# Performance work log

Hardware: AMD Instinct MI355X
Metric: run time of the kernel (lower is better)

Reference implementation:

```python
import jax, jax.numpy as jnp
import numpy as np

N = 100000
E = 3_200_000
H = 64
R = 2
NEG = 0.01   # leaky_relu default slope
EPS = 1e-5   # BatchNorm eps


def leaky(x):
    return jnp.where(x > 0, x, NEG * x)


def bn(x, g, b, m, v):
    # BatchNorm1d in eval mode (running statistics)
    return (x - m) * jax.lax.rsqrt(v + EPS) * g + b


def setup_inputs() -> dict:
    key = jax.random.key(0)
    ks = jax.random.split(key, 16)
    d = {}
    d["des"] = jax.random.normal(ks[0], (N, 768), jnp.float32)
    d["num"] = jax.random.normal(ks[1], (N, 5), jnp.float32)
    d["cat"] = jax.random.normal(ks[2], (N, 6), jnp.float32)
    d["edge_index"] = jax.random.randint(ks[3], (2, E), 0, N)
    d["edge_type"] = jax.random.randint(ks[4], (E,), 0, R)

    def lin(k, o, i):
        return (jax.random.normal(k, (o, i), jnp.float32) / np.float32(np.sqrt(i)))

    # projection heads: Linear + BatchNorm1d params
    d["des_W"] = lin(ks[5], H, 768); d["des_b"] = jnp.zeros((H,), jnp.float32)
    d["num_W"] = lin(ks[6], H, 5);   d["num_b"] = jnp.zeros((H,), jnp.float32)
    d["cat_W"] = lin(ks[7], H, 6);   d["cat_b"] = jnp.zeros((H,), jnp.float32)
    for name, kk in (("des", ks[8]), ("num", ks[9]), ("cat", ks[10])):
        d[name + "_g"] = jnp.ones((H,), jnp.float32)
        d[name + "_beta"] = jnp.zeros((H,), jnp.float32)
        d[name + "_m"] = 0.1 * jax.random.normal(kk, (H,), jnp.float32)
        d[name + "_v"] = jnp.ones((H,), jnp.float32)
    # RGCN relation weights [R, in, out] (used as F.linear(x, W[r]) -> x @ W[r].T)
    d["rgcn_W"] = jax.random.normal(ks[11], (R, H, H), jnp.float32) / np.float32(np.sqrt(H))
    # classifier
    d["cls_W1"] = lin(ks[12], H // 2, H); d["cls_b1"] = jnp.zeros((H // 2,), jnp.float32)
    d["cls_W2"] = lin(ks[13], 2, H // 2); d["cls_b2"] = jnp.zeros((2,), jnp.float32)
    return d


def reference(des, num, cat, edge_index, edge_type,
              des_W, des_b, des_g, des_beta, des_m, des_v,
              num_W, num_b, num_g, num_beta, num_m, num_v,
              cat_W, cat_b, cat_g, cat_beta, cat_m, cat_v,
              rgcn_W, cls_W1, cls_b1, cls_W2, cls_b2):
    # feature fusion: three Linear+BN+LeakyReLU branches summed
    x = leaky(bn(des @ des_W.T + des_b, des_g, des_beta, des_m, des_v))
    x = x + leaky(bn(num @ num_W.T + num_b, num_g, num_beta, num_m, num_v))
    x = x + leaky(bn(cat @ cat_W.T + cat_b, cat_g, cat_beta, cat_m, cat_v))

    # SimpleRGCNConv: per-relation linear transform + masked scatter-mean over edges
    src, dst = edge_index[0], edge_index[1]  # PyG: row=source, col=target
    n = x.shape[0]
    acc = jnp.zeros((n, H), x.dtype)
    for r in range(R):
        x_r = x @ rgcn_W[r].T                       # F.linear(x, weight[r])
        mask = (edge_type == r).astype(x.dtype)     # [E]
        msg = x_r[src] * mask[:, None]              # gather + mask
        s = jax.ops.segment_sum(msg, dst, num_segments=n)
        cnt = jax.ops.segment_sum(mask, dst, num_segments=n)
        acc = acc + s / jnp.maximum(cnt, 1.0)[:, None]  # mean; 0 for isolated nodes
    x = leaky(acc / R)  # mean over relations

    # dropout in eval mode is identity; classifier
    h = leaky(x @ cls_W1.T + cls_b1)
    return h @ cls_W2.T + cls_b2
```

## Files before the change

### kernel.cpp

```cpp
#include <hip/hip_runtime.h>

typedef unsigned int u32;
typedef unsigned short u16;

#define NEG 0.01f
#define BN_EPS 1e-5f

typedef __attribute__((ext_vector_type(8))) short bf16x8;
typedef __attribute__((ext_vector_type(4))) float f32x4;

__device__ __forceinline__ float bl(u32 u){ union { u32 i; float f; } c; c.i = u << 16; return c.f; }
__device__ __forceinline__ float bh(u32 u){ union { u32 i; float f; } c; c.i = u & 0xFFFF0000u; return c.f; }
__device__ __forceinline__ u16 f2b(float f){
  union { float f; u32 i; } c; c.f = f;
  u32 t = c.i + 0x7FFFu + ((c.i >> 16) & 1u);
  return (u16)(t >> 16);
}
__device__ __forceinline__ float leaky(float v){ return v > 0.f ? v : NEG * v; }

__global__ __launch_bounds__(256) void k_hist_prep(
    const int* __restrict__ ei, const int* __restrict__ et, int E, int HB,
    int* __restrict__ deg2,
    const float* __restrict__ desWf, const float* __restrict__ rgcnW,
    const float* __restrict__ W1, u16* __restrict__ tab)
{
  int bid = blockIdx.x;
  if (bid < HB) {
    int e = bid * 256 + threadIdx.x;
    if (e < E) atomicAdd(&deg2[ei[E + e] * 2 + et[e]], 1);
  } else {
    int i = (bid - HB) * 256 + threadIdx.x;
    if (i < 49152) {
      int j = i & 7, lane = (i >> 3) & 63, t = (i >> 9) & 3, k = i >> 11;
      int row = 16 * t + (lane & 15);
      int col = 32 * k + 8 * (lane >> 4) + j;
      tab[i] = f2b(desWf[row * 768 + col]);
    } else if (i < 57344) {
      int j = i - 49152;
      int h = j >> 7, k = j & 127;
      tab[i] = f2b(rgcnW[(k >= 64 ? 4096 : 0) + h * 64 + (k & 63)]);
    } else if (i < 59392) {
      tab[i] = f2b(W1[i - 57344]);
    }
  }
}

__global__ __launch_bounds__(256) void k_fuse_scan(
    const float* __restrict__ des, const float* __restrict__ nump, const float* __restrict__ catp,
    const u16* __restrict__ Wpk, const float* __restrict__ desB,
    const float* __restrict__ numW, const float* __restrict__ numB,
    const float* __restrict__ catW, const float* __restrict__ catB,
    const float* __restrict__ dg, const float* __restrict__ dbe, const float* __restrict__ dm, const float* __restrict__ dv,
    const float* __restrict__ ng, const float* __restrict__ nbe, const float* __restrict__ nm, const float* __restrict__ nv,
    const float* __restrict__ cg, const float* __restrict__ cbe, const float* __restrict__ cm, const float* __restrict__ cv,
    u16* __restrict__ x16, int n,
    const int* __restrict__ deg2, int* __restrict__ offs2, int M)
{
  const int tid  = threadIdx.x;
  const int lane = tid & 63;
  const int w    = tid >> 6;

  if (blockIdx.x == 0) {
    __shared__ int wsum[4];
    __shared__ int carry;
    if (tid == 0) carry = 0;
    __syncthreads();
    for (int base = 0; base < M; base += 1024) {
      int idx = base + tid * 4;
      int4 v = {0, 0, 0, 0};
      if (idx < M) v = *(const int4*)(deg2 + idx);
      int s4 = v.x + v.y + v.z + v.w;
      int s = s4;
      #pragma unroll
      for (int o = 1; o < 64; o <<= 1) { int t = __shfl_up(s, o); if (lane >= o) s += t; }
      if (lane == 63) wsum[w] = s;
      __syncthreads();
      if (tid == 0) {
        int a = wsum[0];
        a += wsum[1]; wsum[1] = a;
        a += wsum[2]; wsum[2] = a;
        a += wsum[3]; wsum[3] = a;
      }
      __syncthreads();
      int wbase = (w == 0) ? 0 : wsum[w - 1];
      int ebase = carry + wbase + (s - s4);
      if (idx < M) {
        int4 o4;
        o4.x = ebase;
        o4.y = ebase + v.x;
        o4.z = ebase + v.x + v.y;
        o4.w = ebase + v.x + v.y + v.z;
        *(int4*)(offs2 + idx) = o4;
      }
      __syncthreads();
      if (tid == 0) carry += wsum[3];
      __syncthreads();
    }
    if (tid == 0) offs2[M] = carry;
    return;
  }

  __shared__ float ync[64][66];
  __shared__ __align__(16) u16 atile[64 * 136];

  const int quad = lane >> 4;
  const int l15  = lane & 15;
  const int fb   = blockIdx.x - 1;
  const int rowbase = fb * 64 + 16 * w;

  {
    float nw[5], cw[6];
    #pragma unroll
    for (int j = 0; j < 5; ++j) nw[j] = numW[lane * 5 + j];
    #pragma unroll
    for (int j = 0; j < 6; ++j) cw[j] = catW[lane * 6 + j];
    float An = ng[lane] * rsqrtf(nv[lane] + BN_EPS);
    float Bn = (numB[lane] - nm[lane]) * An + nbe[lane];
    float Ac = cg[lane] * rsqrtf(cv[lane] + BN_EPS);
    float Bc = (catB[lane] - cm[lane]) * Ac + cbe[lane];
    for (int m = 0; m < 16; ++m) {
      int node = rowbase + m; if (node > n - 1) node = n - 1;
      float yn = 0.f, yc = 0.f;
      #pragma unroll
      for (int j = 0; j < 5; ++j) yn = fmaf(nump[node * 5 + j], nw[j], yn);
      #pragma unroll
      for (int j = 0; j < 6; ++j) yc = fmaf(catp[node * 6 + j], cw[j], yc);
      ync[16 * w + m][lane] = leaky(yn * An + Bn) + leaky(yc * Ac + Bc);
    }
  }

  float Ad4[4], Bd4[4];
  #pragma unroll
  for (int t = 0; t < 4; ++t) {
    int nn = 16 * t + l15;
    float A = dg[nn] * rsqrtf(dv[nn] + BN_EPS);
    Ad4[t] = A;
    Bd4[t] = (desB[nn] - dm[nn]) * A + dbe[nn];
  }
  __syncthreads();

  const u16* bP = Wpk + lane * 8;

  f32x4 acc[4];
  #pragma unroll
  for (int t = 0; t < 4; ++t) acc[t] = (f32x4){0.f, 0.f, 0.f, 0.f};

  const int blk64 = fb * 64;
  for (int tile = 0; tile < 6; ++tile) {
    if (tile > 0) __syncthreads();
    #pragma unroll
    for (int it = 0; it < 4; ++it) {
      int j  = it * 256 + tid;
      int r  = j >> 4;
      int sg = j & 15;
      int row = blk64 + r; if (row > n - 1) row = n - 1;
      const float* p = des + (size_t)row * 768 + tile * 128 + sg * 8;
      float4 u = *(const float4*)p;
      float4 v = *(const float4*)(p + 4);
      u32* d = (u32*)(atile + r * 136 + sg * 8);
      d[0] = (u32)f2b(u.x) | ((u32)f2b(u.y) << 16);
      d[1] = (u32)f2b(u.z) | ((u32)f2b(u.w) << 16);
      d[2] = (u32)f2b(v.x) | ((u32)f2b(v.y) << 16);
      d[3] = (u32)f2b(v.z) | ((u32)f2b(v.w) << 16);
    }
    __syncthreads();
    #pragma unroll
    for (int kk = 0; kk < 4; ++kk) {
      bf16x8 a = *(const bf16x8*)(atile + (16 * w + l15) * 136 + kk * 32 + quad * 8);
      int kg = tile * 4 + kk;
      acc[0] = __builtin_amdgcn_mfma_f32_16x16x32_bf16(a, *(const bf16x8*)(bP + kg * 2048       ), acc[0], 0, 0, 0);
      acc[1] = __builtin_amdgcn_mfma_f32_16x16x32_bf16(a, *(const bf16x8*)(bP + kg * 2048 +  512), acc[1], 0, 0, 0);
      acc[2] = __builtin_amdgcn_mfma_f32_16x16x32_bf16(a, *(const bf16x8*)(bP + kg * 2048 + 1024), acc[2], 0, 0, 0);
      acc[3] = __builtin_amdgcn_mfma_f32_16x16x32_bf16(a, *(const bf16x8*)(bP + kg * 2048 + 1536), acc[3], 0, 0, 0);
    }
  }

  #pragma unroll
  for (int t = 0; t < 4; ++t) {
    #pragma unroll
    for (int r = 0; r < 4; ++r) {
      int m = quad * 4 + r;
      int node = rowbase + m;
      if (node < n) {
        int nn = 16 * t + l15;
        float v = leaky(acc[t][r] * Ad4[t] + Bd4[t]) + ync[16 * w + m][nn];
        x16[(size_t)node * 64 + nn] = f2b(v);
      }
    }
  }
}

__global__ void k_place(const int* __restrict__ ei, const int* __restrict__ et, int E,
                        const int* __restrict__ offs2, int* __restrict__ cur2, int* __restrict__ packed)
{
  int e = blockIdx.x * 256 + threadIdx.x;
  if (e < E) {
    int bin = ei[E + e] * 2 + et[e];
    int pos = offs2[bin] + atomicAdd(&cur2[bin], 1);
    packed[pos] = ei[e];
  }
}

__global__ __launch_bounds__(256) void k_agg(
    const u16* __restrict__ x16, const int* __restrict__ offs2, const int* __restrict__ packed,
    u32* __restrict__ agg, int n)
{
  const int tid = threadIdx.x, lane = tid & 63, w = tid >> 6;
  const int c = lane & 31, half = lane >> 5;

  for (int nd = blockIdx.x * 4 + w; nd < n; nd += gridDim.x * 4) {
    int o0 = offs2[nd * 2], o1 = offs2[nd * 2 + 1], o2 = offs2[nd * 2 + 2];
    float aE[2], aO[2];

    #pragma unroll
    for (int rel = 0; rel < 2; ++rel) {
      int beg = rel ? o1 : o0;
      int end = rel ? o2 : o1;
      float accE = 0.f, accO = 0.f;
      for (int j0 = beg; j0 < end; j0 += 64) {
        int idx = j0 + lane;
        int p = (idx < end) ? packed[idx] : 0;
        p = (p < 0) ? 0 : ((p > n - 1) ? (n - 1) : p);
        int cn = end - j0; if (cn > 64) cn = 64;
        int t = 0;
        for (; t + 16 <= cn; t += 16) {
          int s0 = __shfl(p, t      + half);
          int s1 = __shfl(p, t + 2  + half);
          int s2 = __shfl(p, t + 4  + half);
          int s3 = __shfl(p, t + 6  + half);
          int s4 = __shfl(p, t + 8  + half);
          int s5 = __shfl(p, t + 10 + half);
          int s6 = __shfl(p, t + 12 + half);
          int s7 = __shfl(p, t + 14 + half);
          u32 v0 = *(const u32*)(x16 + (size_t)s0 * 64 + 2 * c);
          u32 v1 = *(const u32*)(x16 + (size_t)s1 * 64 + 2 * c);
          u32 v2 = *(const u32*)(x16 + (size_t)s2 * 64 + 2 * c);
          u32 v3 = *(const u32*)(x16 + (size_t)s3 * 64 + 2 * c);
          u32 v4 = *(const u32*)(x16 + (size_t)s4 * 64 + 2 * c);
          u32 v5 = *(const u32*)(x16 + (size_t)s5 * 64 + 2 * c);
          u32 v6 = *(const u32*)(x16 + (size_t)s6 * 64 + 2 * c);
          u32 v7 = *(const u32*)(x16 + (size_t)s7 * 64 + 2 * c);
          accE += ((bl(v0) + bl(v1)) + (bl(v2) + bl(v3))) + ((bl(v4) + bl(v5)) + (bl(v6) + bl(v7)));
          accO += ((bh(v0) + bh(v1)) + (bh(v2) + bh(v3))) + ((bh(v4) + bh(v5)) + (bh(v6) + bh(v7)));
        }
        for (; t + 8 <= cn; t += 8) {
          int s0 = __shfl(p, t     + half);
          int s1 = __shfl(p, t + 2 + half);
          int s2 = __shfl(p, t + 4 + half);
          int s3 = __shfl(p, t + 6 + half);
          u32 v0 = *(const u32*)(x16 + (size_t)s0 * 64 + 2 * c);
          u32 v1 = *(const u32*)(x16 + (size_t)s1 * 64 + 2 * c);
          u32 v2 = *(const u32*)(x16 + (size_t)s2 * 64 + 2 * c);
          u32 v3 = *(const u32*)(x16 + (size_t)s3 * 64 + 2 * c);
          accE += (bl(v0) + bl(v1)) + (bl(v2) + bl(v3));
          accO += (bh(v0) + bh(v1)) + (bh(v2) + bh(v3));
        }
        for (; t + 2 <= cn; t += 2) {
          int s0 = __shfl(p, t + half);
          u32 v0 = *(const u32*)(x16 + (size_t)s0 * 64 + 2 * c);
          accE += bl(v0); accO += bh(v0);
        }
        if (t < cn) {
          int s0 = __shfl(p, t);
          if (half == 0) {
            u32 v0 = *(const u32*)(x16 + (size_t)s0 * 64 + 2 * c);
            accE += bl(v0); accO += bh(v0);
          }
        }
      }
      accE += __shfl_xor(accE, 32);
      accO += __shfl_xor(accO, 32);
      int cnt = end - beg;
      float sc = 1.f / (float)(cnt > 1 ? cnt : 1);
      aE[rel] = accE * sc;
      aO[rel] = accO * sc;
    }

    float sE = half ? aE[1] : aE[0];
    float sO = half ? aO[1] : aO[0];
    agg[(size_t)nd * 64 + lane] = (u32)f2b(sE) | ((u32)f2b(sO) << 16);
  }
}

__global__ __launch_bounds__(256) void k_mlp(
    const u32* __restrict__ agg, const u16* __restrict__ Wmlp, const u16* __restrict__ W1p,
    const float* __restrict__ b1, const float* __restrict__ W2, const float* __restrict__ b2,
    float2* __restrict__ out, int n)
{
  __shared__ __align__(16) u16 h1[4][16][72];
  __shared__ float h2[4][16][34];

  const int tid = threadIdx.x, lane = tid & 63, w = tid >> 6;
  const int quad = lane >> 4, l15 = lane & 15;
  const int rowbase = blockIdx.x * 64 + 16 * w;

  int rowA = rowbase + l15; if (rowA > n - 1) rowA = n - 1;
  const u16* aRow = (const u16*)(agg + (size_t)rowA * 64);

  f32x4 acc[4];
  #pragma unroll
  for (int t = 0; t < 4; ++t) acc[t] = (f32x4){0.f, 0.f, 0.f, 0.f};
  #pragma unroll
  for (int ks = 0; ks < 4; ++ks) {
    bf16x8 a = *(const bf16x8*)(aRow + ks * 32 + quad * 8);
    #pragma unroll
    for (int t = 0; t < 4; ++t) {
      bf16x8 b = *(const bf16x8*)(Wmlp + (size_t)(16 * t + l15) * 128 + ks * 32 + quad * 8);
      acc[t] = __builtin_amdgcn_mfma_f32_16x16x32_bf16(a, b, acc[t], 0, 0, 0);
    }
  }
  #pragma unroll
  for (int t = 0; t < 4; ++t)
    #pragma unroll
    for (int r = 0; r < 4; ++r) {
      int m = quad * 4 + r;
      h1[w][m][16 * t + l15] = f2b(leaky(0.5f * acc[t][r]));
    }
  __syncthreads();

  f32x4 acc2[2];
  acc2[0] = (f32x4){0.f, 0.f, 0.f, 0.f};
  acc2[1] = (f32x4){0.f, 0.f, 0.f, 0.f};
  #pragma unroll
  for (int ks = 0; ks < 2; ++ks) {
    bf16x8 a = *(const bf16x8*)(&h1[w][l15][ks * 32 + quad * 8]);
    #pragma unroll
    for (int t = 0; t < 2; ++t) {
      bf16x8 b = *(const bf16x8*)(W1p + (size_t)(16 * t + l15) * 64 + ks * 32 + quad * 8);
      acc2[t] = __builtin_amdgcn_mfma_f32_16x16x32_bf16(a, b, acc2[t], 0, 0, 0);
    }
  }
  #pragma unroll
  for (int t = 0; t < 2; ++t)
    #pragma unroll
    for (int r = 0; r < 4; ++r) {
      int m = quad * 4 + r;
      int j = 16 * t + l15;
      h2[w][m][j] = leaky(acc2[t][r] + b1[j]);
    }
  __syncthreads();

  float t0 = 0.f, t1 = 0.f;
  #pragma unroll
  for (int jj = 0; jj < 8; ++jj) {
    int j = quad * 8 + jj;
    float hv = h2[w][l15][j];
    t0 = fmaf(hv, W2[j], t0);
    t1 = fmaf(hv, W2[32 + j], t1);
  }
  t0 += __shfl_xor(t0, 16); t0 += __shfl_xor(t0, 32);
  t1 += __shfl_xor(t1, 16); t1 += __shfl_xor(t1, 32);
  int node = rowbase + l15;
  if (quad == 0 && node < n) {
    float2 q; q.x = t0 + b2[0]; q.y = t1 + b2[1];
    out[node] = q;
  }
}

extern "C" void kernel_launch(void* const* d_in, const int* in_sizes, int n_in,
                              void* d_out, int out_size, void* d_ws, size_t ws_size,
                              hipStream_t stream)
{
  const float* des  = (const float*)d_in[0];
  const float* nump = (const float*)d_in[1];
  const float* catp = (const float*)d_in[2];
  const int* ei   = (const int*)d_in[3];
  const int* et   = (const int*)d_in[4];
  const float* desW = (const float*)d_in[5];
  const float* desB = (const float*)d_in[6];
  const float* numW = (const float*)d_in[7];
  const float* numB = (const float*)d_in[8];
  const float* catW = (const float*)d_in[9];
  const float* catB = (const float*)d_in[10];
  const float* dg  = (const float*)d_in[11];
  const float* dbe = (const float*)d_in[12];
  const float* dm  = (const float*)d_in[13];
  const float* dv  = (const float*)d_in[14];
  const float* ng  = (const float*)d_in[15];
  const float* nbe = (const float*)d_in[16];
  const float* nm  = (const float*)d_in[17];
  const float* nv  = (const float*)d_in[18];
  const float* cg  = (const float*)d_in[19];
  const float* cbe = (const float*)d_in[20];
  const float* cm  = (const float*)d_in[21];
  const float* cv  = (const float*)d_in[22];
  const float* rgcnW = (const float*)d_in[23];
  const float* W1 = (const float*)d_in[24];
  const float* b1 = (const float*)d_in[25];
  const float* W2 = (const float*)d_in[26];
  const float* b2 = (const float*)d_in[27];

  const int N = in_sizes[1] / 5;
  const int E = in_sizes[4];
  const int M = 2 * N;
  const int NB = (N + 63) / 64;

  char* ws = (char*)d_ws;
  u16* tab    = (u16*)ws;                  size_t off = (size_t)59392 * 2;
  off = (off + 255) & ~(size_t)255;
  u16* x16    = (u16*)(ws + off);          off += (size_t)N * 64 * 2;
  u32* agg    = (u32*)(ws + off);          off += (size_t)N * 64 * 4;
  int* deg2   = (int*)(ws + off);          off += (size_t)M * 4;
  int* cur2   = (int*)(ws + off);          off += (size_t)M * 4;
  int* offs2  = (int*)(ws + off);          off += (size_t)(M + 1) * 4;
  off = (off + 255) & ~(size_t)255;
  int* packed = (int*)(ws + off);

  u16* Wpk    = tab;
  u16* Wmlp   = tab + 49152;
  u16* W1p    = tab + 57344;

  hipMemsetAsync(deg2, 0, (size_t)M * 8, stream);

  const int HB = (E + 255) / 256;
  const int PB = (59392 + 255) / 256;
  k_hist_prep<<<HB + PB, 256, 0, stream>>>(ei, et, E, HB, deg2, desW, rgcnW, W1, tab);

  k_fuse_scan<<<NB + 1, 256, 0, stream>>>(des, nump, catp, Wpk, desB, numW, numB, catW, catB,
                                          dg, dbe, dm, dv, ng, nbe, nm, nv, cg, cbe, cm, cv,
                                          x16, N, deg2, offs2, M);

  k_place<<<(E + 255) / 256, 256, 0, stream>>>(ei, et, E, offs2, cur2, packed);
  k_agg<<<2048, 256, 0, stream>>>(x16, offs2, packed, agg, N);
  k_mlp<<<(N + 63) / 64, 256, 0, stream>>>(agg, Wmlp, W1p, b1, W2, b2, (float2*)d_out, N);
}
```

Baseline: 942.0 us.

## Replace single-block serial scan with three-pass multi-block prefix scan

The exclusive prefix scan over per-node, per-relation degree counts used to run in one block that loops serially over 200K entries alongside the fuse kernel. It is now split into three kernels: per-chunk reduction, a single-block scan of the chunk sums, and a per-chunk scan that adds the offsets. This removes a long single-block tail, at the cost of two extra launches and losing overlap with the fuse work. NCH is 196, which fits inside the 256-thread scanB.

```diff
diff --git a/kernel.cpp b/kernel.cpp
--- a/kernel.cpp
+++ b/kernel.cpp
@@ -45,7 +45,80 @@
   }
 }
 
-__global__ __launch_bounds__(256) void k_fuse_scan(
+__global__ __launch_bounds__(256) void k_scanA(
+    const int* __restrict__ deg2, int* __restrict__ psum, int M)
+{
+  __shared__ int ws4[4];
+  const int tid = threadIdx.x, lane = tid & 63, w = tid >> 6;
+  int idx = blockIdx.x * 1024 + tid * 4;
+  int4 v = {0, 0, 0, 0};
+  if (idx < M) v = *(const int4*)(deg2 + idx);
+  int s = v.x + v.y + v.z + v.w;
+  #pragma unroll
+  for (int o = 1; o < 64; o <<= 1) s += __shfl_xor(s, o);
+  if (lane == 0) ws4[w] = s;
+  __syncthreads();
+  if (tid == 0) psum[blockIdx.x] = ws4[0] + ws4[1] + ws4[2] + ws4[3];
+}
+
+__global__ __launch_bounds__(256) void k_scanB(
+    const int* __restrict__ psum, int* __restrict__ poff, int NCH)
+{
+  __shared__ int wsum[4];
+  const int tid = threadIdx.x, lane = tid & 63, w = tid >> 6;
+  int v = (tid < NCH) ? psum[tid] : 0;
+  int s = v;
+  #pragma unroll
+  for (int o = 1; o < 64; o <<= 1) { int t = __shfl_up(s, o); if (lane >= o) s += t; }
+  if (lane == 63) wsum[w] = s;
+  __syncthreads();
+  if (tid == 0) {
+    int a = wsum[0];
+    a += wsum[1]; wsum[1] = a;
+    a += wsum[2]; wsum[2] = a;
+    a += wsum[3]; wsum[3] = a;
+  }
+  __syncthreads();
+  int wbase = (w == 0) ? 0 : wsum[w - 1];
+  if (tid < NCH) poff[tid] = wbase + (s - v);
+}
+
+__global__ __launch_bounds__(256) void k_scanC(
+    const int* __restrict__ deg2, const int* __restrict__ poff,
+    int* __restrict__ offs2, int M, int E)
+{
+  __shared__ int wsum[4];
+  const int tid = threadIdx.x, lane = tid & 63, w = tid >> 6;
+  int idx = blockIdx.x * 1024 + tid * 4;
+  int4 v = {0, 0, 0, 0};
+  if (idx < M) v = *(const int4*)(deg2 + idx);
+  int s4 = v.x + v.y + v.z + v.w;
+  int s = s4;
+  #pragma unroll
+  for (int o = 1; o < 64; o <<= 1) { int t = __shfl_up(s, o); if (lane >= o) s += t; }
+  if (lane == 63) wsum[w] = s;
+  __syncthreads();
+  if (tid == 0) {
+    int a = wsum[0];
+    a += wsum[1]; wsum[1] = a;
+    a += wsum[2]; wsum[2] = a;
+    a += wsum[3]; wsum[3] = a;
+  }
+  __syncthreads();
+  int wbase = (w == 0) ? 0 : wsum[w - 1];
+  int ebase = poff[blockIdx.x] + wbase + (s - s4);
+  if (idx < M) {
+    int4 o4;
+    o4.x = ebase;
+    o4.y = ebase + v.x;
+    o4.z = ebase + v.x + v.y;
+    o4.w = ebase + v.x + v.y + v.z;
+    *(int4*)(offs2 + idx) = o4;
+  }
+  if (blockIdx.x == 0 && tid == 0) offs2[M] = E;
+}
+
+__global__ __launch_bounds__(256) void k_fuse(
     const float* __restrict__ des, const float* __restrict__ nump, const float* __restrict__ catp,
     const u16* __restrict__ Wpk, const float* __restrict__ desB,
     const float* __restrict__ numW, const float* __restrict__ numB,
@@ -53,59 +126,18 @@
     const float* __restrict__ dg, const float* __restrict__ dbe, const float* __restrict__ dm, const float* __restrict__ dv,
     const float* __restrict__ ng, const float* __restrict__ nbe, const float* __restrict__ nm, const float* __restrict__ nv,
     const float* __restrict__ cg, const float* __restrict__ cbe, const float* __restrict__ cm, const float* __restrict__ cv,
-    u16* __restrict__ x16, int n,
-    const int* __restrict__ deg2, int* __restrict__ offs2, int M)
+    u16* __restrict__ x16, int n)
 {
   const int tid  = threadIdx.x;
   const int lane = tid & 63;
   const int w    = tid >> 6;
 
-  if (blockIdx.x == 0) {
-    __shared__ int wsum[4];
-    __shared__ int carry;
-    if (tid == 0) carry = 0;
-    __syncthreads();
-    for (int base = 0; base < M; base += 1024) {
-      int idx = base + tid * 4;
-      int4 v = {0, 0, 0, 0};
-      if (idx < M) v = *(const int4*)(deg2 + idx);
-      int s4 = v.x + v.y + v.z + v.w;
-      int s = s4;
-      #pragma unroll
-      for (int o = 1; o < 64; o <<= 1) { int t = __shfl_up(s, o); if (lane >= o) s += t; }
-      if (lane == 63) wsum[w] = s;
-      __syncthreads();
-      if (tid == 0) {
-        int a = wsum[0];
-        a += wsum[1]; wsum[1] = a;
-        a += wsum[2]; wsum[2] = a;
-        a += wsum[3]; wsum[3] = a;
-      }
-      __syncthreads();
-      int wbase = (w == 0) ? 0 : wsum[w - 1];
-      int ebase = carry + wbase + (s - s4);
-      if (idx < M) {
-        int4 o4;
-        o4.x = ebase;
-        o4.y = ebase + v.x;
-        o4.z = ebase + v.x + v.y;
-        o4.w = ebase + v.x + v.y + v.z;
-        *(int4*)(offs2 + idx) = o4;
-      }
-      __syncthreads();
-      if (tid == 0) carry += wsum[3];
-      __syncthreads();
-    }
-    if (tid == 0) offs2[M] = carry;
-    return;
-  }
-
   __shared__ float ync[64][66];
   __shared__ __align__(16) u16 atile[64 * 136];
 
   const int quad = lane >> 4;
   const int l15  = lane & 15;
-  const int fb   = blockIdx.x - 1;
+  const int fb   = blockIdx.x;
   const int rowbase = fb * 64 + 16 * w;
 
   {
@@ -394,6 +426,7 @@
   const int E = in_sizes[4];
   const int M = 2 * N;
   const int NB = (N + 63) / 64;
+  const int NCH = (M + 1023) / 1024;
 
   char* ws = (char*)d_ws;
   u16* tab    = (u16*)ws;                  size_t off = (size_t)59392 * 2;
@@ -404,6 +437,9 @@
   int* cur2   = (int*)(ws + off);          off += (size_t)M * 4;
   int* offs2  = (int*)(ws + off);          off += (size_t)(M + 1) * 4;
   off = (off + 255) & ~(size_t)255;
+  int* psum   = (int*)(ws + off);          off += (size_t)NCH * 4;
+  int* poff   = (int*)(ws + off);          off += (size_t)NCH * 4;
+  off = (off + 255) & ~(size_t)255;
   int* packed = (int*)(ws + off);
 
   u16* Wpk    = tab;
@@ -416,9 +452,13 @@
   const int PB = (59392 + 255) / 256;
   k_hist_prep<<<HB + PB, 256, 0, stream>>>(ei, et, E, HB, deg2, desW, rgcnW, W1, tab);
 
-  k_fuse_scan<<<NB + 1, 256, 0, stream>>>(des, nump, catp, Wpk, desB, numW, numB, catW, catB,
-                                          dg, dbe, dm, dv, ng, nbe, nm, nv, cg, cbe, cm, cv,
-                                          x16, N, deg2, offs2, M);
+  k_fuse<<<NB, 256, 0, stream>>>(des, nump, catp, Wpk, desB, numW, numB, catW, catB,
+                                 dg, dbe, dm, dv, ng, nbe, nm, nv, cg, cbe, cm, cv,
+                                 x16, N);
+
+  k_scanA<<<NCH, 256, 0, stream>>>(deg2, psum, M);
+  k_scanB<<<1, 256, 0, stream>>>(psum, poff, NCH);
+  k_scanC<<<NCH, 256, 0, stream>>>(deg2, poff, offs2, M, E);
 
   k_place<<<(E + 255) / 256, 256, 0, stream>>>(ei, et, E, offs2, cur2, packed);
   k_agg<<<2048, 256, 0, stream>>>(x16, offs2, packed, agg, N);
```

Measured after the change: 872.4 us. 7.4% less time.
